# Kernel tuning notes

Hardware: AMD Instinct MI355X
Metric: run time of the kernel (lower is better)

## Reference

```python
import jax, jax.numpy as jnp
import numpy as np

N = 100000
E = 1600000
IN_F = 64
HID = 128
GC_OUT = 128
FEATS_OUT = 128


def _init_params(key):
    ks = jax.random.split(key, 6)
    s = 0.02
    return dict(
        W1=jax.random.normal(ks[0], (IN_F, HID), jnp.float32) * s,
        b1=jnp.zeros((HID,), jnp.float32),
        W2=jax.random.normal(ks[1], (HID, HID), jnp.float32) * s,
        b2=jnp.zeros((HID,), jnp.float32),
        Wgc=jax.random.normal(ks[2], (HID + IN_F, GC_OUT), jnp.float32) * s,
        bgc=jnp.zeros((GC_OUT,), jnp.float32),
        Wc=jax.random.normal(ks[3], (HID + GC_OUT, FEATS_OUT), jnp.float32) * s,
        bc=jnp.zeros((FEATS_OUT,), jnp.float32),
    )


def setup_inputs() -> dict:
    key = jax.random.key(0)
    k_f, k_e, k_p = jax.random.split(key, 3)
    inp = dict(
        feats=jax.random.normal(k_f, (N, IN_F), jnp.float32),
        edges=jax.random.randint(k_e, (2, E), 0, N, jnp.int64 if jax.config.read('jax_enable_x64') else jnp.int32),
        batch=jnp.zeros((N,), jnp.int32),
    )
    inp.update(_init_params(k_p))
    return inp


def _gcn_conv(x, edges, Wgc, bgc):
    # PyG GCNConv: linear transform, add self-loops, symmetric deg norm, scatter-add.
    n = x.shape[0]
    x = x @ Wgc  # [N, GC_OUT]
    loop = jnp.arange(n, dtype=edges.dtype)
    src = jnp.concatenate([edges[0], loop])
    dst = jnp.concatenate([edges[1], loop])
    deg = jax.ops.segment_sum(jnp.ones_like(dst, dtype=x.dtype), dst, num_segments=n)
    dinv = jnp.where(deg > 0, jax.lax.rsqrt(deg), 0.0)
    norm = dinv[src] * dinv[dst]  # [E+N]
    msg = x[src] * norm[:, None]  # gather + scale (memory-bound)
    agg = jax.ops.segment_sum(msg, dst, num_segments=n)  # scatter-add
    return agg + bgc


def reference(feats, edges, batch, W1, b1, W2, b2, Wgc, bgc, Wc, bc):
    elu = jax.nn.elu
    nfeats = elu(elu(feats @ W1 + b1) @ W2 + b2)  # fcnn
    gc_in = jnp.concatenate([nfeats, feats], axis=1)  # inject_input_to_gc
    gc_feats = _gcn_conv(gc_in, edges, Wgc, bgc)
    out_feats = elu(jnp.concatenate([nfeats, gc_feats], axis=1) @ Wc + bc)
    return (out_feats, edges, batch)
```

## Files before the change

### kernel.cpp

```cpp
#include <hip/hip_runtime.h>
#include <hip/hip_bf16.h>
#include <hip/hip_fp8.h>

constexpr int NN = 100000;
constexpr int NE = 1600000;

constexpr int SH1  = 9;
constexpr int NB1  = (NN + 511) >> SH1;
constexpr int EB   = 8192;
constexpr int NBLK = (NE + EB - 1) / EB;
constexpr int NH   = NB1 * NBLK;

constexpr float FP8_SCL  = 128.f;
constexpr float FP8_ISCL = 1.f / 128.f;

typedef __bf16 bf16_t;
typedef bf16_t bf16x8 __attribute__((ext_vector_type(8)));
typedef bf16_t bf16x4 __attribute__((ext_vector_type(4)));
typedef float  f32x4  __attribute__((ext_vector_type(4)));

__device__ inline float elu_fast(float v) {
  return v > 0.f ? v : (__expf(v) - 1.f);
}

__device__ inline unsigned char f_to_fp8(float v) {
  __hip_fp8_e4m3 q(v);
  return q.__x;
}
template<int SEL>
__device__ inline float fp8_to_f(unsigned int word) {
#if __has_builtin(__builtin_amdgcn_cvt_f32_fp8)
  return __builtin_amdgcn_cvt_f32_fp8(word, SEL);
#else
  __hip_fp8_e4m3 t; t.__x = (word >> (8 * SEL)) & 0xff; return (float)t;
#endif
}
__device__ inline void fp8x8_fma(float* acc, uint2 v, float s) {
  acc[0] += fp8_to_f<0>(v.x) * s;
  acc[1] += fp8_to_f<1>(v.x) * s;
  acc[2] += fp8_to_f<2>(v.x) * s;
  acc[3] += fp8_to_f<3>(v.x) * s;
  acc[4] += fp8_to_f<0>(v.y) * s;
  acc[5] += fp8_to_f<1>(v.y) * s;
  acc[6] += fp8_to_f<2>(v.y) * s;
  acc[7] += fp8_to_f<3>(v.y) * s;
}

constexpr int SB = 256;

__global__ void scan_blk(const int* __restrict__ in, int* __restrict__ incl,
                         int* __restrict__ bsum, int n) {
  __shared__ int sm[SB];
  int i = blockIdx.x * SB + threadIdx.x;
  int v = (i < n) ? in[i] : 0;
  sm[threadIdx.x] = v;
  __syncthreads();
  for (int off = 1; off < SB; off <<= 1) {
    int t = (threadIdx.x >= off) ? sm[threadIdx.x - off] : 0;
    __syncthreads();
    sm[threadIdx.x] += t;
    __syncthreads();
  }
  if (i < n) incl[i] = sm[threadIdx.x];
  if (threadIdx.x == SB - 1) bsum[blockIdx.x] = sm[SB - 1];
}

__global__ void scan_top(int* __restrict__ bsum, int nb) {
  __shared__ int sm[512];
  int t = threadIdx.x;
  int v = (t < nb) ? bsum[t] : 0;
  sm[t] = v;
  __syncthreads();
  for (int off = 1; off < 512; off <<= 1) {
    int u = (t >= off) ? sm[t - off] : 0;
    __syncthreads();
    sm[t] += u;
    __syncthreads();
  }
  if (t < nb) bsum[t] = sm[t] - v;
}

__global__ void scan_add(const int* __restrict__ incl, const int* __restrict__ in,
                         const int* __restrict__ bsum, int* __restrict__ outoff, int n) {
  int i = blockIdx.x * SB + threadIdx.x;
  if (i < n) {
    int off = bsum[blockIdx.x];
    outoff[i] = off + incl[i] - in[i];
    if (i == n - 1) outoff[n] = off + incl[i];
  }
}


__global__ __launch_bounds__(256) void histA(const int* __restrict__ dst,
                                             int* __restrict__ H, int e) {
  __shared__ int h[NB1];
  for (int i = threadIdx.x; i < NB1; i += 256) h[i] = 0;
  __syncthreads();
  int base = blockIdx.x * EB;
  int end = min(base + EB, e);
  for (int i = base + threadIdx.x; i < end; i += 256)
    atomicAdd(&h[dst[i] >> SH1], 1);
  __syncthreads();
  for (int i = threadIdx.x; i < NB1; i += 256)
    H[i * NBLK + blockIdx.x] = h[i];
}

__global__ void boff_k(const int* __restrict__ Hoff, int* __restrict__ boff) {
  int i = blockIdx.x * blockDim.x + threadIdx.x;
  if (i < NB1) boff[i] = Hoff[i * NBLK];
  if (i == NB1) boff[NB1] = NE;
}

__global__ __launch_bounds__(256) void scatterA(
    const int* __restrict__ src, const int* __restrict__ dst,
    const int* __restrict__ Hoff, unsigned long long* __restrict__ ebuf, int e) {
  __shared__ int cur[NB1];
  for (int i = threadIdx.x; i < NB1; i += 256)
    cur[i] = Hoff[i * NBLK + blockIdx.x];
  __syncthreads();
  int base = blockIdx.x * EB;
  int end = min(base + EB, e);
  for (int i = base + threadIdx.x; i < end; i += 256) {
    int d = dst[i], s = src[i];
    int pos = atomicAdd(&cur[d >> SH1], 1);
    ebuf[pos] = ((unsigned long long)(unsigned)d << 32) | (unsigned)s;
  }
}


__global__ __launch_bounds__(512) void bfin(const unsigned long long* __restrict__ ebuf,
                                            const int* __restrict__ boff,
                                            int* __restrict__ row_off, float* __restrict__ dinv,
                                            int* __restrict__ csr, int n) {
  __shared__ int cnt[512];
  __shared__ int loc[512];
  const int tid = threadIdx.x;
  const int b = blockIdx.x;
  cnt[tid] = 0;
  __syncthreads();
  const int e0 = boff[b], e1 = boff[b + 1];
  for (int e = e0 + tid; e < e1; e += 512)
    atomicAdd(&cnt[(int)(ebuf[e] >> 32) & 511], 1);
  __syncthreads();
  loc[tid] = cnt[tid];
  __syncthreads();
  for (int off = 1; off < 512; off <<= 1) {
    int t = (tid >= off) ? loc[tid - off] : 0;
    __syncthreads();
    loc[tid] += t;
    __syncthreads();
  }
  const int excl = loc[tid] - cnt[tid];
  const int node = (b << SH1) + tid;
  if (node < n) {
    row_off[node] = boff[b] + excl;
    dinv[node] = rsqrtf((float)cnt[tid] + 1.0f);
  }
  if (b == NB1 - 1 && tid == 0) row_off[n] = NE;
  cnt[tid] = boff[b] + excl;
  __syncthreads();
  for (int e = e0 + tid; e < e1; e += 512) {
    unsigned long long v = ebuf[e];
    int dl = (int)(v >> 32) & 511;
    int s  = (int)(v & 0xffffffffu);
    int slot = atomicAdd(&cnt[dl], 1);
    csr[slot] = s;
  }
}


__global__ void i2f_k(const int* __restrict__ in, float* __restrict__ out, int n) {
  int i = blockIdx.x * blockDim.x + threadIdx.x;
  if (i < n) out[i] = (float)in[i];
}

__global__ void wprep4(const float* __restrict__ W1, const float* __restrict__ W2,
                       const float* __restrict__ Wgc, const float* __restrict__ Wc,
                       bf16_t* __restrict__ Wf) {
  int idx = blockIdx.x * blockDim.x + threadIdx.x;
  const float* W; int base;
  if      (idx < 8192)  { W = W1;  base = 0; }
  else if (idx < 24576) { W = W2;  base = 8192; }
  else if (idx < 49152) { W = Wgc; base = 24576; }
  else                  { W = Wc;  base = 49152; }
  int il   = idx - base;
  int j    = il & 7;
  int lane = (il >> 3) & 63;
  int c    = (il >> 9) & 7;
  int kt   = il >> 12;
  int k    = kt * 32 + (lane >> 4) * 8 + j;
  int col  = c * 16 + (lane & 15);
  Wf[idx] = (bf16_t)W[(size_t)k * 128 + col];
}

__global__ __launch_bounds__(256) void mf_dense123(
    const float* __restrict__ A, const bf16_t* __restrict__ W1f, const float* __restrict__ b1,
    const bf16_t* __restrict__ W2f, const float* __restrict__ b2,
    const bf16_t* __restrict__ Wgf,
    bf16_t* __restrict__ h2out, unsigned char* __restrict__ xqout, int n)
{
  __shared__ __align__(16) char h1s[64 * 256];
  const int tid  = threadIdx.x;
  const int wv   = tid >> 6;
  const int lane = tid & 63;
  const int r    = lane & 15;
  const int kb   = lane >> 4;
  const int row0 = blockIdx.x * 64 + wv * 16;

  const bf16x8* W1V = (const bf16x8*)W1f;
  const bf16x8* W2V = (const bf16x8*)W2f;
  const bf16x8* WgV = (const bf16x8*)Wgf;

  f32x4 acc[8];
  #pragma unroll
  for (int c = 0; c < 8; ++c) acc[c] = (f32x4){0.f, 0.f, 0.f, 0.f};

  #pragma unroll
  for (int kt = 0; kt < 2; ++kt) {
    const int kofs = kt * 32 + kb * 8;
    int row = row0 + r; if (row >= n) row = n - 1;
    const float* fp = A + (size_t)row * 64 + kofs;
    float4 u = *(const float4*)fp;
    float4 v = *(const float4*)(fp + 4);
    bf16x8 a = (bf16x8){(bf16_t)u.x, (bf16_t)u.y, (bf16_t)u.z, (bf16_t)u.w,
                        (bf16_t)v.x, (bf16_t)v.y, (bf16_t)v.z, (bf16_t)v.w};
    #pragma unroll
    for (int c = 0; c < 8; ++c) {
      bf16x8 b = W1V[(kt * 8 + c) * 64 + lane];
      acc[c] = __builtin_amdgcn_mfma_f32_16x16x32_bf16(a, b, acc[c], 0, 0, 0);
    }
  }

  #pragma unroll
  for (int c = 0; c < 8; ++c) {
    const int col = c * 16 + r;
    const float bv = b1[col];
    #pragma unroll
    for (int q = 0; q < 4; ++q) {
      int rloc = wv * 16 + kb * 4 + q;
      float v = elu_fast(acc[c][q] + bv);
      int off = (rloc * 256 + col * 2) ^ ((rloc & 7) << 4);
      *(bf16_t*)(h1s + off) = (bf16_t)v;
    }
  }

  #pragma unroll
  for (int c = 0; c < 8; ++c) acc[c] = (f32x4){0.f, 0.f, 0.f, 0.f};

  #pragma unroll
  for (int kt = 0; kt < 4; ++kt) {
    const int kbyte = (kt * 32 + kb * 8) * 2;
    int rloc = wv * 16 + r;
    int off = (rloc * 256 + kbyte) ^ ((rloc & 7) << 4);
    bf16x8 a = *(const bf16x8*)(h1s + off);
    #pragma unroll
    for (int c = 0; c < 8; ++c) {
      bf16x8 b = W2V[(kt * 8 + c) * 64 + lane];
      acc[c] = __builtin_amdgcn_mfma_f32_16x16x32_bf16(a, b, acc[c], 0, 0, 0);
    }
  }

  #pragma unroll
  for (int c = 0; c < 8; ++c) {
    const int col = c * 16 + r;
    const float bv = b2[col];
    #pragma unroll
    for (int q = 0; q < 4; ++q) {
      int row  = row0 + kb * 4 + q;
      int rloc = wv * 16 + kb * 4 + q;
      float v = elu_fast(acc[c][q] + bv);
      int off = (rloc * 256 + col * 2) ^ ((rloc & 7) << 4);
      *(bf16_t*)(h1s + off) = (bf16_t)v;
      if (row < n) h2out[(size_t)row * 128 + col] = (bf16_t)v;
    }
  }

  #pragma unroll
  for (int c = 0; c < 8; ++c) acc[c] = (f32x4){0.f, 0.f, 0.f, 0.f};

  #pragma unroll
  for (int kt = 0; kt < 6; ++kt) {
    const int kofs = kt * 32 + kb * 8;
    bf16x8 a;
    if (kofs < 128) {
      int rloc = wv * 16 + r;
      int off = (rloc * 256 + kofs * 2) ^ ((rloc & 7) << 4);
      a = *(const bf16x8*)(h1s + off);
    } else {
      int row = row0 + r; if (row >= n) row = n - 1;
      const float* fp = A + (size_t)row * 64 + (kofs - 128);
      float4 u = *(const float4*)fp;
      float4 v = *(const float4*)(fp + 4);
      a = (bf16x8){(bf16_t)u.x, (bf16_t)u.y, (bf16_t)u.z, (bf16_t)u.w,
                   (bf16_t)v.x, (bf16_t)v.y, (bf16_t)v.z, (bf16_t)v.w};
    }
    #pragma unroll
    for (int c = 0; c < 8; ++c) {
      bf16x8 b = WgV[(kt * 8 + c) * 64 + lane];
      acc[c] = __builtin_amdgcn_mfma_f32_16x16x32_bf16(a, b, acc[c], 0, 0, 0);
    }
  }

  #pragma unroll
  for (int c = 0; c < 8; ++c) {
    const int col = c * 16 + r;
    #pragma unroll
    for (int q = 0; q < 4; ++q) {
      int row = row0 + kb * 4 + q;
      if (row < n)
        xqout[(size_t)row * 128 + col] = f_to_fp8(acc[c][q] * FP8_SCL);
    }
  }
}

template<int K1, int K2, bool DOELU, int OMODE>
__global__ __launch_bounds__(256) void mf_dense(
    const bf16_t* __restrict__ A1, const bf16_t* __restrict__ A2b,
    const bf16_t* __restrict__ Wf, const float* __restrict__ bias,
    bf16_t* __restrict__ outb, float* __restrict__ outf, int n)
{
  constexpr int K   = K1 + K2;
  constexpr int NKT = K / 32;

  const int tid  = threadIdx.x;
  const int wv   = tid >> 6;
  const int lane = tid & 63;
  const int r    = lane & 15;
  const int kb   = lane >> 4;
  const int row0 = blockIdx.x * 64 + wv * 16;

  f32x4 acc[8];
  #pragma unroll
  for (int c = 0; c < 8; ++c) acc[c] = (f32x4){0.f, 0.f, 0.f, 0.f};

  const bf16x8* WfV = (const bf16x8*)Wf;

  #pragma unroll
  for (int kt = 0; kt < NKT; ++kt) {
    const int kofs = kt * 32 + kb * 8;
    int row = row0 + r; if (row >= n) row = n - 1;
    bf16x8 a;
    if (kofs < K1) a = *(const bf16x8*)(A1 + (size_t)row * K1 + kofs);
    else           a = *(const bf16x8*)(A2b + (size_t)row * K2 + (kofs - K1));
    #pragma unroll
    for (int c = 0; c < 8; ++c) {
      bf16x8 b = WfV[(kt * 8 + c) * 64 + lane];
      acc[c] = __builtin_amdgcn_mfma_f32_16x16x32_bf16(a, b, acc[c], 0, 0, 0);
    }
  }

  #pragma unroll
  for (int c = 0; c < 8; ++c) {
    const int col = c * 16 + r;
    const float bv = bias ? bias[col] : 0.f;
    #pragma unroll
    for (int q = 0; q < 4; ++q) {
      int row = row0 + kb * 4 + q;
      if (row < n) {
        float v = acc[c][q] + bv;
        if (DOELU) v = elu_fast(v);
        if (OMODE == 0) outb[(size_t)row * 128 + col] = (bf16_t)v;
        else            outf[(size_t)row * 128 + col] = v;
      }
    }
  }
}

__global__ __launch_bounds__(256) void gcn_agg5(
    const int* __restrict__ row_off, const int* __restrict__ csr,
    const float* __restrict__ dinv, const unsigned char* __restrict__ xq,
    const float* __restrict__ bgc, bf16_t* __restrict__ agg, int n)
{
  int w = (int)((blockIdx.x * (unsigned)blockDim.x + threadIdx.x) >> 6);
  if (w >= n) return;
  const int lane = threadIdx.x & 63;
  const int g  = lane >> 4;
  const int li = lane & 15;

  const float dd = dinv[w];
  float acc[8];
  #pragma unroll
  for (int j = 0; j < 8; ++j) acc[j] = 0.f;

  if (g == 0) {
    uint2 sv = ((const uint2*)(xq + (size_t)w * 128))[li];
    fp8x8_fma(acc, sv, dd);
  }

  const int e0 = row_off[w], e1 = row_off[w + 1];
  int e = e0;
  for (; e + 16 <= e1; e += 16) {
    #pragma unroll
    for (int u = 0; u < 4; ++u) {
      int s = csr[e + 4 * u + g];
      float ds = dinv[s];
      uint2 v = ((const uint2*)(xq + (size_t)s * 128))[li];
      fp8x8_fma(acc, v, ds);
    }
  }
  for (; e < e1; e += 4) {
    int idx = e + g;
    int cidx = idx < e1 ? idx : e1 - 1;
    int s = csr[cidx];
    float ds = idx < e1 ? dinv[s] : 0.f;
    uint2 v = ((const uint2*)(xq + (size_t)s * 128))[li];
    fp8x8_fma(acc, v, ds);
  }

  #pragma unroll
  for (int j = 0; j < 8; ++j) {
    acc[j] += __shfl_xor(acc[j], 16);
    acc[j] += __shfl_xor(acc[j], 32);
  }

  if (g == 0) {
    const float sc = dd * FP8_ISCL;
    f32x4 b0 = ((const f32x4*)bgc)[2 * li];
    f32x4 b1 = ((const f32x4*)bgc)[2 * li + 1];
    bf16x8 o;
    o[0] = (bf16_t)(acc[0] * sc + b0[0]); o[1] = (bf16_t)(acc[1] * sc + b0[1]);
    o[2] = (bf16_t)(acc[2] * sc + b0[2]); o[3] = (bf16_t)(acc[3] * sc + b0[3]);
    o[4] = (bf16_t)(acc[4] * sc + b1[0]); o[5] = (bf16_t)(acc[5] * sc + b1[1]);
    o[6] = (bf16_t)(acc[6] * sc + b1[2]); o[7] = (bf16_t)(acc[7] * sc + b1[3]);
    ((bf16x8*)(agg + (size_t)w * 128))[li] = o;
  }
}


extern "C" void kernel_launch(void* const* d_in, const int* in_sizes, int n_in,
                              void* d_out, int out_size, void* d_ws, size_t ws_size,
                              hipStream_t stream) {
  (void)in_sizes; (void)n_in; (void)out_size; (void)ws_size;
  const float* feats = (const float*)d_in[0];
  const int*   edges = (const int*)d_in[1];
  const int*   batch = (const int*)d_in[2];
  const float* W1  = (const float*)d_in[3];
  const float* b1  = (const float*)d_in[4];
  const float* W2  = (const float*)d_in[5];
  const float* b2  = (const float*)d_in[6];
  const float* Wgc = (const float*)d_in[7];
  const float* bgc = (const float*)d_in[8];
  const float* Wc  = (const float*)d_in[9];
  const float* bc  = (const float*)d_in[10];
  float* out = (float*)d_out;

  bf16_t* h2b  = (bf16_t*)d_ws;
  bf16_t* aggb = h2b  + (size_t)NN * 128;
  unsigned char* xq8 = (unsigned char*)(aggb + (size_t)NN * 128);
  float*  dinv = (float*)(xq8 + (size_t)NN * 128);
  bf16_t* wall = (bf16_t*)(dinv + NN);
  bf16_t* w1f  = wall;
  bf16_t* w2f  = wall + 8192;
  bf16_t* wgcf = wall + 24576;
  bf16_t* wcf  = wall + 49152;

  int* scr     = (int*)d_out;
  int* csr_src = scr;
  int* row_off = csr_src + NE;
  int* H       = row_off + NN + 1;
  int* Hincl   = H + NH;
  int* Hoff    = Hincl + NH;
  int* boff    = Hoff + NH + 1;
  int* bsum2   = boff + NB1 + 1;
  unsigned long long* ebuf =
      (unsigned long long*)(((uintptr_t)(bsum2 + 512) + 7) & ~(uintptr_t)7);

  const int* esrc = edges;
  const int* edst = edges + NE;

  const int nscH = (NH + SB - 1) / SB;

  histA   <<<NBLK, 256, 0, stream>>>(edst, H, NE);
  scan_blk<<<nscH, SB, 0, stream>>>(H, Hincl, bsum2, NH);
  scan_top<<<1, 512, 0, stream>>>(bsum2, nscH);
  scan_add<<<nscH, SB, 0, stream>>>(Hincl, H, bsum2, Hoff, NH);
  boff_k  <<<1, 256, 0, stream>>>(Hoff, boff);
  scatterA<<<NBLK, 256, 0, stream>>>(esrc, edst, Hoff, ebuf, NE);
  bfin    <<<NB1, 512, 0, stream>>>(ebuf, boff, row_off, dinv, csr_src, NN);

  wprep4<<<320, 256, 0, stream>>>(W1, W2, Wgc, Wc, wall);

  const int nb = (NN + 63) / 64;
  mf_dense123<<<nb, 256, 0, stream>>>(feats, w1f, b1, w2f, b2, wgcf, h2b, xq8, NN);

  long long wthreads = (long long)NN * 64;
  gcn_agg5<<<(int)((wthreads + 255) / 256), 256, 0, stream>>>(
      row_off, csr_src, dinv, xq8, bgc, aggb, NN);

  mf_dense<128, 128, true, 1><<<nb, 256, 0, stream>>>(
      h2b, aggb, wcf, bc, nullptr, out, NN);

  size_t off = (size_t)NN * 128;
  i2f_k<<<(2 * NE + 255) / 256, 256, 0, stream>>>(edges, out + off, 2 * NE);
  i2f_k<<<(NN + 255) / 256, 256, 0, stream>>>(batch, out + off + (size_t)2 * NE, NN);
}
```

Before: 205.5 us.

## Process two row tiles per wave in fused dense kernel and use packed fp8 conversion

The fused three-layer dense kernel now handles 128 rows per block, with each wave computing two 16-row tiles. Each loaded weight fragment is reused for two MFMAs, halving weight loads per row. This doubles the accumulator registers and shared memory, which may lower occupancy. Separately, the fp8 decode in the aggregation uses a packed two-value conversion builtin instead of four single-value conversions.

```diff
diff --git a/kernel.cpp b/kernel.cpp
--- a/kernel.cpp
+++ b/kernel.cpp
@@ -18,6 +18,7 @@
 typedef bf16_t bf16x8 __attribute__((ext_vector_type(8)));
 typedef bf16_t bf16x4 __attribute__((ext_vector_type(4)));
 typedef float  f32x4  __attribute__((ext_vector_type(4)));
+typedef float  f32x2  __attribute__((ext_vector_type(2)));
 
 __device__ inline float elu_fast(float v) {
   return v > 0.f ? v : (__expf(v) - 1.f);
@@ -35,15 +36,23 @@
   __hip_fp8_e4m3 t; t.__x = (word >> (8 * SEL)) & 0xff; return (float)t;
 #endif
 }
+template<bool W>
+__device__ inline f32x2 fp8pk2(unsigned int word) {
+#if __has_builtin(__builtin_amdgcn_cvt_pk_f32_fp8)
+  return __builtin_amdgcn_cvt_pk_f32_fp8((int)word, W);
+#else
+  f32x2 o; o.x = fp8_to_f<W ? 2 : 0>(word); o.y = fp8_to_f<W ? 3 : 1>(word); return o;
+#endif
+}
 __device__ inline void fp8x8_fma(float* acc, uint2 v, float s) {
-  acc[0] += fp8_to_f<0>(v.x) * s;
-  acc[1] += fp8_to_f<1>(v.x) * s;
-  acc[2] += fp8_to_f<2>(v.x) * s;
-  acc[3] += fp8_to_f<3>(v.x) * s;
-  acc[4] += fp8_to_f<0>(v.y) * s;
-  acc[5] += fp8_to_f<1>(v.y) * s;
-  acc[6] += fp8_to_f<2>(v.y) * s;
-  acc[7] += fp8_to_f<3>(v.y) * s;
+  f32x2 p0 = fp8pk2<false>(v.x);
+  f32x2 p1 = fp8pk2<true >(v.x);
+  f32x2 p2 = fp8pk2<false>(v.y);
+  f32x2 p3 = fp8pk2<true >(v.y);
+  acc[0] += p0.x * s; acc[1] += p0.y * s;
+  acc[2] += p1.x * s; acc[3] += p1.y * s;
+  acc[4] += p2.x * s; acc[5] += p2.y * s;
+  acc[6] += p3.x * s; acc[7] += p3.y * s;
 }
 
 constexpr int SB = 256;
@@ -199,35 +208,47 @@
     const bf16_t* __restrict__ Wgf,
     bf16_t* __restrict__ h2out, unsigned char* __restrict__ xqout, int n)
 {
-  __shared__ __align__(16) char h1s[64 * 256];
+  __shared__ __align__(16) char h1s[128 * 256];
   const int tid  = threadIdx.x;
   const int wv   = tid >> 6;
   const int lane = tid & 63;
   const int r    = lane & 15;
   const int kb   = lane >> 4;
-  const int row0 = blockIdx.x * 64 + wv * 16;
+  const int lrow0 = wv * 16;
+  const int lrow1 = 64 + wv * 16;
+  const int grow0 = blockIdx.x * 128 + lrow0;
+  const int grow1 = blockIdx.x * 128 + lrow1;
 
   const bf16x8* W1V = (const bf16x8*)W1f;
   const bf16x8* W2V = (const bf16x8*)W2f;
   const bf16x8* WgV = (const bf16x8*)Wgf;
 
-  f32x4 acc[8];
-  #pragma unroll
-  for (int c = 0; c < 8; ++c) acc[c] = (f32x4){0.f, 0.f, 0.f, 0.f};
+  f32x4 acc0[8], acc1[8];
+
+  #pragma unroll
+  for (int c = 0; c < 8; ++c) {
+    acc0[c] = (f32x4){0.f, 0.f, 0.f, 0.f};
+    acc1[c] = (f32x4){0.f, 0.f, 0.f, 0.f};
+  }
 
   #pragma unroll
   for (int kt = 0; kt < 2; ++kt) {
     const int kofs = kt * 32 + kb * 8;
-    int row = row0 + r; if (row >= n) row = n - 1;
-    const float* fp = A + (size_t)row * 64 + kofs;
-    float4 u = *(const float4*)fp;
-    float4 v = *(const float4*)(fp + 4);
-    bf16x8 a = (bf16x8){(bf16_t)u.x, (bf16_t)u.y, (bf16_t)u.z, (bf16_t)u.w,
-                        (bf16_t)v.x, (bf16_t)v.y, (bf16_t)v.z, (bf16_t)v.w};
+    int g0 = grow0 + r; if (g0 >= n) g0 = n - 1;
+    int g1 = grow1 + r; if (g1 >= n) g1 = n - 1;
+    const float* fp0 = A + (size_t)g0 * 64 + kofs;
+    const float* fp1 = A + (size_t)g1 * 64 + kofs;
+    float4 u0 = *(const float4*)fp0, v0 = *(const float4*)(fp0 + 4);
+    float4 u1 = *(const float4*)fp1, v1 = *(const float4*)(fp1 + 4);
+    bf16x8 a0 = (bf16x8){(bf16_t)u0.x, (bf16_t)u0.y, (bf16_t)u0.z, (bf16_t)u0.w,
+                         (bf16_t)v0.x, (bf16_t)v0.y, (bf16_t)v0.z, (bf16_t)v0.w};
+    bf16x8 a1 = (bf16x8){(bf16_t)u1.x, (bf16_t)u1.y, (bf16_t)u1.z, (bf16_t)u1.w,
+                         (bf16_t)v1.x, (bf16_t)v1.y, (bf16_t)v1.z, (bf16_t)v1.w};
     #pragma unroll
     for (int c = 0; c < 8; ++c) {
       bf16x8 b = W1V[(kt * 8 + c) * 64 + lane];
-      acc[c] = __builtin_amdgcn_mfma_f32_16x16x32_bf16(a, b, acc[c], 0, 0, 0);
+      acc0[c] = __builtin_amdgcn_mfma_f32_16x16x32_bf16(a0, b, acc0[c], 0, 0, 0);
+      acc1[c] = __builtin_amdgcn_mfma_f32_16x16x32_bf16(a1, b, acc1[c], 0, 0, 0);
     }
   }
 
@@ -237,26 +258,37 @@
     const float bv = b1[col];
     #pragma unroll
     for (int q = 0; q < 4; ++q) {
-      int rloc = wv * 16 + kb * 4 + q;
-      float v = elu_fast(acc[c][q] + bv);
-      int off = (rloc * 256 + col * 2) ^ ((rloc & 7) << 4);
-      *(bf16_t*)(h1s + off) = (bf16_t)v;
-    }
-  }
-
-  #pragma unroll
-  for (int c = 0; c < 8; ++c) acc[c] = (f32x4){0.f, 0.f, 0.f, 0.f};
+      int rl0 = lrow0 + kb * 4 + q;
+      int rl1 = lrow1 + kb * 4 + q;
+      float v0 = elu_fast(acc0[c][q] + bv);
+      float v1 = elu_fast(acc1[c][q] + bv);
+      int off0 = (rl0 * 256 + col * 2) ^ ((rl0 & 7) << 4);
+      int off1 = (rl1 * 256 + col * 2) ^ ((rl1 & 7) << 4);
+      *(bf16_t*)(h1s + off0) = (bf16_t)v0;
+      *(bf16_t*)(h1s + off1) = (bf16_t)v1;
+    }
+  }
+
+  #pragma unroll
+  for (int c = 0; c < 8; ++c) {
+    acc0[c] = (f32x4){0.f, 0.f, 0.f, 0.f};
+    acc1[c] = (f32x4){0.f, 0.f, 0.f, 0.f};
+  }
 
   #pragma unroll
   for (int kt = 0; kt < 4; ++kt) {
     const int kbyte = (kt * 32 + kb * 8) * 2;
-    int rloc = wv * 16 + r;
-    int off = (rloc * 256 + kbyte) ^ ((rloc & 7) << 4);
-    bf16x8 a = *(const bf16x8*)(h1s + off);
+    int rl0 = lrow0 + r;
+    int rl1 = lrow1 + r;
+    int off0 = (rl0 * 256 + kbyte) ^ ((rl0 & 7) << 4);
+    int off1 = (rl1 * 256 + kbyte) ^ ((rl1 & 7) << 4);
+    bf16x8 a0 = *(const bf16x8*)(h1s + off0);
+    bf16x8 a1 = *(const bf16x8*)(h1s + off1);
     #pragma unroll
     for (int c = 0; c < 8; ++c) {
       bf16x8 b = W2V[(kt * 8 + c) * 64 + lane];
-      acc[c] = __builtin_amdgcn_mfma_f32_16x16x32_bf16(a, b, acc[c], 0, 0, 0);
+      acc0[c] = __builtin_amdgcn_mfma_f32_16x16x32_bf16(a0, b, acc0[c], 0, 0, 0);
+      acc1[c] = __builtin_amdgcn_mfma_f32_16x16x32_bf16(a1, b, acc1[c], 0, 0, 0);
     }
   }
 
@@ -266,38 +298,52 @@
     const float bv = b2[col];
     #pragma unroll
     for (int q = 0; q < 4; ++q) {
-      int row  = row0 + kb * 4 + q;
-      int rloc = wv * 16 + kb * 4 + q;
-      float v = elu_fast(acc[c][q] + bv);
-      int off = (rloc * 256 + col * 2) ^ ((rloc & 7) << 4);
-      *(bf16_t*)(h1s + off) = (bf16_t)v;
-      if (row < n) h2out[(size_t)row * 128 + col] = (bf16_t)v;
-    }
-  }
-
-  #pragma unroll
-  for (int c = 0; c < 8; ++c) acc[c] = (f32x4){0.f, 0.f, 0.f, 0.f};
+      int rl0 = lrow0 + kb * 4 + q, g0 = grow0 + kb * 4 + q;
+      int rl1 = lrow1 + kb * 4 + q, g1 = grow1 + kb * 4 + q;
+      float v0 = elu_fast(acc0[c][q] + bv);
+      float v1 = elu_fast(acc1[c][q] + bv);
+      int off0 = (rl0 * 256 + col * 2) ^ ((rl0 & 7) << 4);
+      int off1 = (rl1 * 256 + col * 2) ^ ((rl1 & 7) << 4);
+      *(bf16_t*)(h1s + off0) = (bf16_t)v0;
+      *(bf16_t*)(h1s + off1) = (bf16_t)v1;
+      if (g0 < n) h2out[(size_t)g0 * 128 + col] = (bf16_t)v0;
+      if (g1 < n) h2out[(size_t)g1 * 128 + col] = (bf16_t)v1;
+    }
+  }
+
+  #pragma unroll
+  for (int c = 0; c < 8; ++c) {
+    acc0[c] = (f32x4){0.f, 0.f, 0.f, 0.f};
+    acc1[c] = (f32x4){0.f, 0.f, 0.f, 0.f};
+  }
 
   #pragma unroll
   for (int kt = 0; kt < 6; ++kt) {
     const int kofs = kt * 32 + kb * 8;
-    bf16x8 a;
+    bf16x8 a0, a1;
     if (kofs < 128) {
-      int rloc = wv * 16 + r;
-      int off = (rloc * 256 + kofs * 2) ^ ((rloc & 7) << 4);
-      a = *(const bf16x8*)(h1s + off);
+      int rl0 = lrow0 + r, rl1 = lrow1 + r;
+      int off0 = (rl0 * 256 + kofs * 2) ^ ((rl0 & 7) << 4);
+      int off1 = (rl1 * 256 + kofs * 2) ^ ((rl1 & 7) << 4);
+      a0 = *(const bf16x8*)(h1s + off0);
+      a1 = *(const bf16x8*)(h1s + off1);
     } else {
-      int row = row0 + r; if (row >= n) row = n - 1;
-      const float* fp = A + (size_t)row * 64 + (kofs - 128);
-      float4 u = *(const float4*)fp;
-      float4 v = *(const float4*)(fp + 4);
-      a = (bf16x8){(bf16_t)u.x, (bf16_t)u.y, (bf16_t)u.z, (bf16_t)u.w,
-                   (bf16_t)v.x, (bf16_t)v.y, (bf16_t)v.z, (bf16_t)v.w};
+      int g0 = grow0 + r; if (g0 >= n) g0 = n - 1;
+      int g1 = grow1 + r; if (g1 >= n) g1 = n - 1;
+      const float* fp0 = A + (size_t)g0 * 64 + (kofs - 128);
+      const float* fp1 = A + (size_t)g1 * 64 + (kofs - 128);
+      float4 u0 = *(const float4*)fp0, v0 = *(const float4*)(fp0 + 4);
+      float4 u1 = *(const float4*)fp1, v1 = *(const float4*)(fp1 + 4);
+      a0 = (bf16x8){(bf16_t)u0.x, (bf16_t)u0.y, (bf16_t)u0.z, (bf16_t)u0.w,
+                    (bf16_t)v0.x, (bf16_t)v0.y, (bf16_t)v0.z, (bf16_t)v0.w};
+      a1 = (bf16x8){(bf16_t)u1.x, (bf16_t)u1.y, (bf16_t)u1.z, (bf16_t)u1.w,
+                    (bf16_t)v1.x, (bf16_t)v1.y, (bf16_t)v1.z, (bf16_t)v1.w};
     }
     #pragma unroll
     for (int c = 0; c < 8; ++c) {
       bf16x8 b = WgV[(kt * 8 + c) * 64 + lane];
-      acc[c] = __builtin_amdgcn_mfma_f32_16x16x32_bf16(a, b, acc[c], 0, 0, 0);
+      acc0[c] = __builtin_amdgcn_mfma_f32_16x16x32_bf16(a0, b, acc0[c], 0, 0, 0);
+      acc1[c] = __builtin_amdgcn_mfma_f32_16x16x32_bf16(a1, b, acc1[c], 0, 0, 0);
     }
   }
 
@@ -306,9 +352,10 @@
     const int col = c * 16 + r;
     #pragma unroll
     for (int q = 0; q < 4; ++q) {
-      int row = row0 + kb * 4 + q;
-      if (row < n)
-        xqout[(size_t)row * 128 + col] = f_to_fp8(acc[c][q] * FP8_SCL);
+      int g0 = grow0 + kb * 4 + q;
+      int g1 = grow1 + kb * 4 + q;
+      if (g0 < n) xqout[(size_t)g0 * 128 + col] = f_to_fp8(acc0[c][q] * FP8_SCL);
+      if (g1 < n) xqout[(size_t)g1 * 128 + col] = f_to_fp8(acc1[c][q] * FP8_SCL);
     }
   }
 }
@@ -480,13 +527,14 @@
 
   wprep4<<<320, 256, 0, stream>>>(W1, W2, Wgc, Wc, wall);
 
-  const int nb = (NN + 63) / 64;
-  mf_dense123<<<nb, 256, 0, stream>>>(feats, w1f, b1, w2f, b2, wgcf, h2b, xq8, NN);
+  const int nb2 = (NN + 127) / 128;
+  mf_dense123<<<nb2, 256, 0, stream>>>(feats, w1f, b1, w2f, b2, wgcf, h2b, xq8, NN);
 
   long long wthreads = (long long)NN * 64;
   gcn_agg5<<<(int)((wthreads + 255) / 256), 256, 0, stream>>>(
       row_off, csr_src, dinv, xq8, bgc, aggb, NN);
 
+  const int nb = (NN + 63) / 64;
   mf_dense<128, 128, true, 1><<<nb, 256, 0, stream>>>(
       h2b, aggb, wcf, bc, nullptr, out, NN);
 
```

Measured after the change: 219.2 us. 1.07x slower.

## Fold source-node degree norm into FP8 quantization, vectorize int-to-float copies

Applied to the files above, without the earlier changes.

Pre-scales each transformed node row by its dinv before FP8 quantization in the dense kernel, so the aggregation kernel no longer gathers dinv[src] per edge and just sums FP8 rows. It also uses packed FP8-to-f32 conversion and vectorizes the edge/batch int-to-float output copies with int4/float4. Scaling by dinv before quantization changes the FP8 value distribution and may shift accuracy. The float4 path assumes the element counts are divisible by 4 and the output offsets are 16-byte aligned.

```diff
diff --git a/kernel.cpp b/kernel.cpp
--- a/kernel.cpp
+++ b/kernel.cpp
@@ -18,6 +18,7 @@
 typedef bf16_t bf16x8 __attribute__((ext_vector_type(8)));
 typedef bf16_t bf16x4 __attribute__((ext_vector_type(4)));
 typedef float  f32x4  __attribute__((ext_vector_type(4)));
+typedef float  f32x2  __attribute__((ext_vector_type(2)));
 
 __device__ inline float elu_fast(float v) {
   return v > 0.f ? v : (__expf(v) - 1.f);
@@ -35,15 +36,33 @@
   __hip_fp8_e4m3 t; t.__x = (word >> (8 * SEL)) & 0xff; return (float)t;
 #endif
 }
+template<bool W>
+__device__ inline f32x2 fp8pk2(unsigned int word) {
+#if __has_builtin(__builtin_amdgcn_cvt_pk_f32_fp8)
+  return __builtin_amdgcn_cvt_pk_f32_fp8((int)word, W);
+#else
+  f32x2 o; o.x = fp8_to_f<W ? 2 : 0>(word); o.y = fp8_to_f<W ? 3 : 1>(word); return o;
+#endif
+}
+__device__ inline void fp8x8_add(float* acc, uint2 v) {
+  f32x2 p0 = fp8pk2<false>(v.x);
+  f32x2 p1 = fp8pk2<true >(v.x);
+  f32x2 p2 = fp8pk2<false>(v.y);
+  f32x2 p3 = fp8pk2<true >(v.y);
+  acc[0] += p0.x; acc[1] += p0.y;
+  acc[2] += p1.x; acc[3] += p1.y;
+  acc[4] += p2.x; acc[5] += p2.y;
+  acc[6] += p3.x; acc[7] += p3.y;
+}
 __device__ inline void fp8x8_fma(float* acc, uint2 v, float s) {
-  acc[0] += fp8_to_f<0>(v.x) * s;
-  acc[1] += fp8_to_f<1>(v.x) * s;
-  acc[2] += fp8_to_f<2>(v.x) * s;
-  acc[3] += fp8_to_f<3>(v.x) * s;
-  acc[4] += fp8_to_f<0>(v.y) * s;
-  acc[5] += fp8_to_f<1>(v.y) * s;
-  acc[6] += fp8_to_f<2>(v.y) * s;
-  acc[7] += fp8_to_f<3>(v.y) * s;
+  f32x2 p0 = fp8pk2<false>(v.x);
+  f32x2 p1 = fp8pk2<true >(v.x);
+  f32x2 p2 = fp8pk2<false>(v.y);
+  f32x2 p3 = fp8pk2<true >(v.y);
+  acc[0] += p0.x * s; acc[1] += p0.y * s;
+  acc[2] += p1.x * s; acc[3] += p1.y * s;
+  acc[4] += p2.x * s; acc[5] += p2.y * s;
+  acc[6] += p3.x * s; acc[7] += p3.y * s;
 }
 
 constexpr int SB = 256;
@@ -169,9 +188,12 @@
 }
 
 
-__global__ void i2f_k(const int* __restrict__ in, float* __restrict__ out, int n) {
+__global__ void i2f4_k(const int4* __restrict__ in, float4* __restrict__ out, int n4) {
   int i = blockIdx.x * blockDim.x + threadIdx.x;
-  if (i < n) out[i] = (float)in[i];
+  if (i < n4) {
+    int4 v = in[i];
+    out[i] = make_float4((float)v.x, (float)v.y, (float)v.z, (float)v.w);
+  }
 }
 
 __global__ void wprep4(const float* __restrict__ W1, const float* __restrict__ W2,
@@ -196,7 +218,7 @@
 __global__ __launch_bounds__(256) void mf_dense123(
     const float* __restrict__ A, const bf16_t* __restrict__ W1f, const float* __restrict__ b1,
     const bf16_t* __restrict__ W2f, const float* __restrict__ b2,
-    const bf16_t* __restrict__ Wgf,
+    const bf16_t* __restrict__ Wgf, const float* __restrict__ dinv_g,
     bf16_t* __restrict__ h2out, unsigned char* __restrict__ xqout, int n)
 {
   __shared__ __align__(16) char h1s[64 * 256];
@@ -301,6 +323,12 @@
     }
   }
 
+  float dv[4];
+  #pragma unroll
+  for (int q = 0; q < 4; ++q) {
+    int row = row0 + kb * 4 + q;
+    dv[q] = (row < n) ? dinv_g[row] * FP8_SCL : 0.f;
+  }
   #pragma unroll
   for (int c = 0; c < 8; ++c) {
     const int col = c * 16 + r;
@@ -308,7 +336,7 @@
     for (int q = 0; q < 4; ++q) {
       int row = row0 + kb * 4 + q;
       if (row < n)
-        xqout[(size_t)row * 128 + col] = f_to_fp8(acc[c][q] * FP8_SCL);
+        xqout[(size_t)row * 128 + col] = f_to_fp8(acc[c][q] * dv[q]);
     }
   }
 }
@@ -366,7 +394,7 @@
   }
 }
 
-__global__ __launch_bounds__(256) void gcn_agg5(
+__global__ __launch_bounds__(256) void gcn_agg6(
     const int* __restrict__ row_off, const int* __restrict__ csr,
     const float* __restrict__ dinv, const unsigned char* __restrict__ xq,
     const float* __restrict__ bgc, bf16_t* __restrict__ agg, int n)
@@ -377,14 +405,13 @@
   const int g  = lane >> 4;
   const int li = lane & 15;
 
-  const float dd = dinv[w];
   float acc[8];
   #pragma unroll
   for (int j = 0; j < 8; ++j) acc[j] = 0.f;
 
   if (g == 0) {
     uint2 sv = ((const uint2*)(xq + (size_t)w * 128))[li];
-    fp8x8_fma(acc, sv, dd);
+    fp8x8_add(acc, sv);
   }
 
   const int e0 = row_off[w], e1 = row_off[w + 1];
@@ -393,18 +420,17 @@
     #pragma unroll
     for (int u = 0; u < 4; ++u) {
       int s = csr[e + 4 * u + g];
-      float ds = dinv[s];
       uint2 v = ((const uint2*)(xq + (size_t)s * 128))[li];
-      fp8x8_fma(acc, v, ds);
+      fp8x8_add(acc, v);
     }
   }
   for (; e < e1; e += 4) {
     int idx = e + g;
     int cidx = idx < e1 ? idx : e1 - 1;
     int s = csr[cidx];
-    float ds = idx < e1 ? dinv[s] : 0.f;
+    float coef = idx < e1 ? 1.f : 0.f;
     uint2 v = ((const uint2*)(xq + (size_t)s * 128))[li];
-    fp8x8_fma(acc, v, ds);
+    fp8x8_fma(acc, v, coef);
   }
 
   #pragma unroll
@@ -414,7 +440,7 @@
   }
 
   if (g == 0) {
-    const float sc = dd * FP8_ISCL;
+    const float sc = dinv[w] * FP8_ISCL;
     f32x4 b0 = ((const f32x4*)bgc)[2 * li];
     f32x4 b1 = ((const f32x4*)bgc)[2 * li + 1];
     bf16x8 o;
@@ -481,16 +507,18 @@
   wprep4<<<320, 256, 0, stream>>>(W1, W2, Wgc, Wc, wall);
 
   const int nb = (NN + 63) / 64;
-  mf_dense123<<<nb, 256, 0, stream>>>(feats, w1f, b1, w2f, b2, wgcf, h2b, xq8, NN);
+  mf_dense123<<<nb, 256, 0, stream>>>(feats, w1f, b1, w2f, b2, wgcf, dinv, h2b, xq8, NN);
 
   long long wthreads = (long long)NN * 64;
-  gcn_agg5<<<(int)((wthreads + 255) / 256), 256, 0, stream>>>(
+  gcn_agg6<<<(int)((wthreads + 255) / 256), 256, 0, stream>>>(
       row_off, csr_src, dinv, xq8, bgc, aggb, NN);
 
   mf_dense<128, 128, true, 1><<<nb, 256, 0, stream>>>(
       h2b, aggb, wcf, bc, nullptr, out, NN);
 
   size_t off = (size_t)NN * 128;
-  i2f_k<<<(2 * NE + 255) / 256, 256, 0, stream>>>(edges, out + off, 2 * NE);
-  i2f_k<<<(NN + 255) / 256, 256, 0, stream>>>(batch, out + off + (size_t)2 * NE, NN);
-}
+  i2f4_k<<<(2 * NE / 4 + 255) / 256, 256, 0, stream>>>(
+      (const int4*)edges, (float4*)(out + off), 2 * NE / 4);
+  i2f4_k<<<(NN / 4 + 255) / 256, 256, 0, stream>>>(
+      (const int4*)batch, (float4*)(out + off + (size_t)2 * NE), NN / 4);
+}
```

Result: no change. 203.0 us (-1.3%).
